# Performance work log

Hardware: AMD Instinct MI355X
Metric: run time of the kernel (lower is better)

## Reference

```python
import jax, jax.numpy as jnp
import numpy as np

N, E, F_IN, EDGE_DIM = 50000, 1600000, 128, 16
H, C = 4, 32            # heads, per-head channels for conv1/conv2
C_OUT = 2               # conv3: heads=1, out_channels=2
HC = H * C              # 128 = hidden_channels * heads
NEG_SLOPE = 0.2
BN_EPS = 1e-5


def setup_inputs() -> dict:
    key = jax.random.key(0)
    ks = jax.random.split(key, 40)
    rn = lambda k, s, sc: jax.random.normal(k, s, jnp.float32) * sc
    inp = {}
    inp["x"] = rn(ks[0], (N, F_IN), 1.0)
    inp["edge_index"] = jax.random.randint(ks[1], (2, E), 0, N, dtype=jnp.int32)
    inp["edge_attr"] = rn(ks[2], (E, EDGE_DIM), 1.0)
    # GATConv layer 1 (in=F_IN -> H x C)
    inp["W1"] = rn(ks[3], (F_IN, HC), F_IN ** -0.5)
    inp["as1"] = rn(ks[4], (H, C), 0.1)
    inp["ad1"] = rn(ks[5], (H, C), 0.1)
    inp["We1"] = rn(ks[6], (EDGE_DIM, HC), EDGE_DIM ** -0.5)
    inp["ae1"] = rn(ks[7], (H, C), 0.1)
    inp["b1"] = jnp.zeros((HC,), jnp.float32)
    # BN1 (eval mode: running stats)
    inp["g1"] = jnp.ones((HC,), jnp.float32)
    inp["be1"] = jnp.zeros((HC,), jnp.float32)
    inp["rm1"] = rn(ks[8], (HC,), 0.1)
    inp["rv1"] = jnp.ones((HC,), jnp.float32)
    # GATConv layer 2 (in=HC -> H x C)
    inp["W2"] = rn(ks[9], (HC, HC), HC ** -0.5)
    inp["as2"] = rn(ks[10], (H, C), 0.1)
    inp["ad2"] = rn(ks[11], (H, C), 0.1)
    inp["We2"] = rn(ks[12], (EDGE_DIM, HC), EDGE_DIM ** -0.5)
    inp["ae2"] = rn(ks[13], (H, C), 0.1)
    inp["b2"] = jnp.zeros((HC,), jnp.float32)
    inp["g2"] = jnp.ones((HC,), jnp.float32)
    inp["be2"] = jnp.zeros((HC,), jnp.float32)
    inp["rm2"] = rn(ks[14], (HC,), 0.1)
    inp["rv2"] = jnp.ones((HC,), jnp.float32)
    inp["W3"] = rn(ks[15], (HC, C_OUT), HC ** -0.5)
    inp["as3"] = rn(ks[16], (1, C_OUT), 0.1)
    inp["ad3"] = rn(ks[17], (1, C_OUT), 0.1)
    inp["We3"] = rn(ks[18], (EDGE_DIM, C_OUT), EDGE_DIM ** -0.5)
    inp["ae3"] = rn(ks[19], (1, C_OUT), 0.1)
    inp["b3"] = jnp.zeros((C_OUT,), jnp.float32)
    return inp


def _gat_layer(x, src, dst, eattr, W, a_s, a_d, We, a_e, b, heads, ch):
    """PyG GATConv (shared src/dst linear, edge_dim, add_self_loops already applied)."""
    n = x.shape[0]
    xp = (x @ W).reshape(n, heads, ch)                      # [N,H,C]
    alpha_src = (xp * a_s).sum(-1)                          # [N,H]
    alpha_dst = (xp * a_d).sum(-1)                          # [N,H]
    ep = (eattr @ We).reshape(-1, heads, ch)                # [E,H,C]
    alpha_e = (ep * a_e).sum(-1)                            # [E,H]
    alpha = alpha_src[src] + alpha_dst[dst] + alpha_e       # [E,H]
    alpha = jax.nn.leaky_relu(alpha, NEG_SLOPE)
    # segment softmax over incoming edges of each dst node
    m = jax.ops.segment_max(alpha, dst, num_segments=n)     # every node has a self loop
    ex = jnp.exp(alpha - m[dst])
    s = jax.ops.segment_sum(ex, dst, num_segments=n)
    alpha = ex / (s[dst] + 1e-16)                           # [E,H]
    msg = xp[src] * alpha[..., None]                        # [E,H,C]
    out = jax.ops.segment_sum(msg, dst, num_segments=n)     # [N,H,C]
    return out.reshape(n, heads * ch) + b


def _bn_eval(x, g, b, rm, rv):
    return (x - rm) * (g * jax.lax.rsqrt(rv + BN_EPS)) + b


def reference(x, edge_index, edge_attr,
              W1, as1, ad1, We1, ae1, b1, g1, be1, rm1, rv1,
              W2, as2, ad2, We2, ae2, b2, g2, be2, rm2, rv2,
              W3, as3, ad3, We3, ae3, b3):
    n = x.shape[0]
    loop = jnp.arange(n, dtype=edge_index.dtype)
    src = jnp.concatenate([edge_index[0], loop])
    dst = jnp.concatenate([edge_index[1], loop])
    # self-loop edge_attr fill_value='mean' (PyG default)
    ea_mean = jnp.broadcast_to(edge_attr.mean(0), (n, edge_attr.shape[1]))
    ea = jnp.concatenate([edge_attr, ea_mean], axis=0)

    h = _gat_layer(x, src, dst, ea, W1, as1, ad1, We1, ae1, b1, H, C)
    h = jax.nn.elu(_bn_eval(h, g1, be1, rm1, rv1))
    h = _gat_layer(h, src, dst, ea, W2, as2, ad2, We2, ae2, b2, H, C)
    h = jax.nn.elu(_bn_eval(h, g2, be2, rm2, rv2))
    out = _gat_layer(h, src, dst, ea, W3, as3, ad3, We3, ae3, b3, 1, C_OUT)
    return out
```

## Files before the change

kernel.cpp:

```cpp
#include <hip/hip_runtime.h>
#include <hip/hip_fp16.h>
#include <math.h>

#define NN 50000
#define EE 1600000
#define ETOT (EE + NN)
#define NEG_SLOPE 0.2f
#define BN_EPS 1e-5f
#define PAY_BLOCKS 1024
#define NPB 128
#define NBUCK ((NN + NPB - 1) / NPB)
#define CHUNK 8192
#define NCHUNK ((EE + CHUNK - 1) / CHUNK)


static __device__ inline unsigned pkh2(float a, float b) {
  __half ha = __float2half_rn(a), hb = __float2half_rn(b);
  unsigned short ua = *(unsigned short*)&ha, ub = *(unsigned short*)&hb;
  return ((unsigned)ub << 16) | ua;
}
static __device__ inline float upkh(unsigned u, int hi) {
  unsigned short s = hi ? (unsigned short)(u >> 16) : (unsigned short)(u & 0xffff);
  __half h = *(__half*)&s;
  return __half2float(h);
}

__global__ void compute_M_k(const float* __restrict__ We1, const float* __restrict__ ae1,
                            const float* __restrict__ We2, const float* __restrict__ ae2,
                            const float* __restrict__ We3, const float* __restrict__ ae3,
                            float* __restrict__ M) {
  int t = threadIdx.x;
  if (t < 64) {
    int d = t >> 2, h = t & 3;
    float s1 = 0.f, s2 = 0.f;
    for (int c = 0; c < 32; ++c) {
      s1 += We1[d * 128 + h * 32 + c] * ae1[h * 32 + c];
      s2 += We2[d * 128 + h * 32 + c] * ae2[h * 32 + c];
    }
    M[t] = s1;
    M[64 + t] = s2;
  }
  if (t < 16) {
    M[128 + t] = We3[t * 2] * ae3[0] + We3[t * 2 + 1] * ae3[1];
  }
}

__global__ __launch_bounds__(256) void payload_k(const int* __restrict__ src,
                                                 const float* __restrict__ ea,
                                                 const float* __restrict__ M,
                                                 uint4* __restrict__ payA,
                                                 uint2* __restrict__ payB,
                                                 float* __restrict__ mean_part) {
  __shared__ float sM[144];
  int t = threadIdx.x;
  if (t < 144) sM[t] = M[t];
  __syncthreads();
  float macc[16];
#pragma unroll
  for (int d = 0; d < 16; ++d) macc[d] = 0.f;

  for (int e = blockIdx.x * 256 + t; e < EE; e += PAY_BLOCKS * 256) {
    float v[16];
    const float4* p = (const float4*)(ea + (size_t)e * 16);
    float4 q0 = p[0], q1 = p[1], q2 = p[2], q3 = p[3];
    v[0] = q0.x; v[1] = q0.y; v[2] = q0.z; v[3] = q0.w;
    v[4] = q1.x; v[5] = q1.y; v[6] = q1.z; v[7] = q1.w;
    v[8] = q2.x; v[9] = q2.y; v[10] = q2.z; v[11] = q2.w;
    v[12] = q3.x; v[13] = q3.y; v[14] = q3.z; v[15] = q3.w;
    float a1[4], a2[4];
#pragma unroll
    for (int h = 0; h < 4; ++h) {
      float s1 = 0.f, s2 = 0.f;
#pragma unroll
      for (int d = 0; d < 16; ++d) {
        s1 += v[d] * sM[d * 4 + h];
        s2 += v[d] * sM[64 + d * 4 + h];
      }
      a1[h] = s1; a2[h] = s2;
    }
    float a3 = 0.f;
#pragma unroll
    for (int d = 0; d < 16; ++d) a3 += v[d] * sM[128 + d];
#pragma unroll
    for (int d = 0; d < 16; ++d) macc[d] += v[d];

    payA[e] = make_uint4(pkh2(a1[0], a1[1]), pkh2(a1[2], a1[3]),
                         pkh2(a2[0], a2[1]), pkh2(a2[2], a2[3]));
    payB[e] = make_uint2(__float_as_uint(a3), (unsigned)src[e]);
  }
#pragma unroll
  for (int d = 0; d < 16; ++d) {
#pragma unroll
    for (int off = 32; off; off >>= 1) macc[d] += __shfl_xor(macc[d], off, 64);
  }
  __shared__ float swsum[4][16];
  int w = t >> 6, l = t & 63;
  if (l == 0) {
#pragma unroll
    for (int d = 0; d < 16; ++d) swsum[w][d] = macc[d];
  }
  __syncthreads();
  if (t < 16) {
    mean_part[(size_t)blockIdx.x * 16 + t] =
        swsum[0][t] + swsum[1][t] + swsum[2][t] + swsum[3][t];
  }
}

__global__ __launch_bounds__(256) void selfloop_k(const float* __restrict__ mean_part,
                                                  const float* __restrict__ M,
                                                  float* __restrict__ alpha_sl) {
  __shared__ float s[256];
  int t = threadIdx.x;
  int d = t & 15, c = t >> 4;
  float v = 0.f;
  for (int i = c * 64; i < (c + 1) * 64; ++i) v += mean_part[(size_t)i * 16 + d];
  s[t] = v;
  __syncthreads();
  if (t < 16) {
    float sum = 0.f;
    for (int c2 = 0; c2 < 16; ++c2) sum += s[c2 * 16 + t];
    s[t] = sum / (float)EE;
  }
  __syncthreads();
  if (t < 9) {
    float r = 0.f;
    if (t < 4) {
      for (int dd = 0; dd < 16; ++dd) r += s[dd] * M[dd * 4 + t];
    } else if (t < 8) {
      int h = t - 4;
      for (int dd = 0; dd < 16; ++dd) r += s[dd] * M[64 + dd * 4 + h];
    } else {
      for (int dd = 0; dd < 16; ++dd) r += s[dd] * M[128 + dd];
    }
    alpha_sl[t] = r;
  }
}

__global__ __launch_bounds__(256) void bcount_k(const int* __restrict__ dst,
                                                int* __restrict__ bucketCnt) {
  __shared__ int hist[512];
  int t = threadIdx.x;
  for (int b = t; b < 512; b += 256) hist[b] = 0;
  __syncthreads();
  for (int e = (blockIdx.x * 256 + t) * 4; e < EE; e += gridDim.x * 1024) {
    int4 d4 = *(const int4*)&dst[e];
    atomicAdd(&hist[d4.x >> 7], 1);
    atomicAdd(&hist[d4.y >> 7], 1);
    atomicAdd(&hist[d4.z >> 7], 1);
    atomicAdd(&hist[d4.w >> 7], 1);
  }
  __syncthreads();
  for (int b = t; b < NBUCK; b += 256)
    if (hist[b]) atomicAdd(&bucketCnt[b], hist[b]);
}

__global__ __launch_bounds__(512) void bscan_k(const int* __restrict__ bucketCnt,
                                               int* __restrict__ pBase,
                                               int* __restrict__ rBase,
                                               int* __restrict__ bcur) {
  __shared__ int s1[512], s2[512];
  int t = threadIdx.x;
  int cnt = (t < NBUCK) ? bucketCnt[t] : 0;
  int nn = 0;
  if (t < NBUCK) {
    int n0 = t * NPB;
    nn = NN - n0; if (nn > NPB) nn = NPB;
  }
  s1[t] = cnt;
  s2[t] = cnt + nn;
  __syncthreads();
  for (int off = 1; off < 512; off <<= 1) {
    int a = (t >= off) ? s1[t - off] : 0;
    int b = (t >= off) ? s2[t - off] : 0;
    __syncthreads();
    s1[t] += a; s2[t] += b;
    __syncthreads();
  }
  if (t < NBUCK) {
    pBase[t] = s1[t] - cnt;
    rBase[t] = s2[t] - (cnt + nn);
    bcur[t] = s1[t] - cnt;
  }
  if (t == 0) { pBase[NBUCK] = EE; rBase[NBUCK] = ETOT; }
}

__global__ __launch_bounds__(256) void bscat_k(const int* __restrict__ dst,
                                               int* __restrict__ bcur,
                                               unsigned* __restrict__ pairs) {
  __shared__ int hist[512];
  __shared__ int ofs[512];
  int t = threadIdx.x;
  for (int c = blockIdx.x; c < NCHUNK; c += gridDim.x) {
    int cb = c * CHUNK;
    for (int b = t; b < 512; b += 256) hist[b] = 0;
    __syncthreads();
#pragma unroll
    for (int k = 0; k < 8; ++k) {
      int e = cb + k * 1024 + t * 4;
      if (e < EE) {
        int4 d4 = *(const int4*)&dst[e];
        atomicAdd(&hist[d4.x >> 7], 1);
        atomicAdd(&hist[d4.y >> 7], 1);
        atomicAdd(&hist[d4.z >> 7], 1);
        atomicAdd(&hist[d4.w >> 7], 1);
      }
    }
    __syncthreads();
    for (int b = t; b < NBUCK; b += 256) {
      int h = hist[b];
      ofs[b] = h ? atomicAdd(&bcur[b], h) : 0;
      hist[b] = 0;
    }
    __syncthreads();
#pragma unroll
    for (int k = 0; k < 8; ++k) {
      int e = cb + k * 1024 + t * 4;
      if (e < EE) {
        int4 d4 = *(const int4*)&dst[e];
        int dd[4] = {d4.x, d4.y, d4.z, d4.w};
#pragma unroll
        for (int j = 0; j < 4; ++j) {
          int b = dd[j] >> 7;
          int pos = ofs[b] + atomicAdd(&hist[b], 1);
          pairs[pos] = ((unsigned)(dd[j] & (NPB - 1)) << 21) | (unsigned)(e + j);
        }
      }
    }
    __syncthreads();
  }
}

__global__ __launch_bounds__(256) void cbuild_k(const int* __restrict__ pBase,
                                                const int* __restrict__ rBase,
                                                const unsigned* __restrict__ pairs,
                                                const uint4* __restrict__ payA,
                                                const uint2* __restrict__ payB,
                                                const float* __restrict__ asl,
                                                uint2* __restrict__ recAE1,
                                                uint2* __restrict__ recAE2,
                                                float* __restrict__ rec3,
                                                int* __restrict__ recSrc,
                                                int* __restrict__ row_ofs) {
  __shared__ int lcnt[NPB];
  __shared__ int ss[NPB];
  __shared__ int cur[NPB];
  int b = blockIdx.x;
  int t = threadIdx.x;
  int n0 = b * NPB;
  int n1 = n0 + NPB; if (n1 > NN) n1 = NN;
  int nn = n1 - n0;
  int pb = pBase[b], pe = pBase[b + 1];
  if (t < NPB) lcnt[t] = 0;
  __syncthreads();
  for (int i = pb + t; i < pe; i += 256) atomicAdd(&lcnt[pairs[i] >> 21], 1);
  __syncthreads();
  int v = (t < nn) ? (lcnt[t] + 1) : 0;
  if (t < NPB) ss[t] = v;
  __syncthreads();
  for (int off = 1; off < NPB; off <<= 1) {
    int a = (t >= off && t < NPB) ? ss[t - off] : 0;
    __syncthreads();
    if (t < NPB) ss[t] += a;
    __syncthreads();
  }
  uint2 a1s = make_uint2(pkh2(asl[0], asl[1]), pkh2(asl[2], asl[3]));
  uint2 a2s = make_uint2(pkh2(asl[4], asl[5]), pkh2(asl[6], asl[7]));
  float a3s = asl[8];
  int rb = rBase[b];
  if (t < nn) {
    int self = rb + ss[t] - v;
    row_ofs[n0 + t] = self;
    cur[t] = self + 1;
    recAE1[self] = a1s; recAE2[self] = a2s; rec3[self] = a3s; recSrc[self] = n0 + t;
  }
  if (b == NBUCK - 1 && t == 0) row_ofs[NN] = ETOT;
  __syncthreads();
  for (int i0 = pb + t; i0 < pe; i0 += 1024) {
    unsigned u[4];
    bool valid[4];
    uint4 pA[4]; uint2 pB[4];
    int pos[4];
#pragma unroll
    for (int k = 0; k < 4; ++k) {
      int i = i0 + k * 256;
      valid[k] = (i < pe);
      if (valid[k]) u[k] = pairs[i];
    }
#pragma unroll
    for (int k = 0; k < 4; ++k) {
      if (valid[k]) {
        int eid = u[k] & 0x1FFFFF;
        pA[k] = payA[eid];
        pB[k] = payB[eid];
        pos[k] = atomicAdd(&cur[u[k] >> 21], 1);
      }
    }
#pragma unroll
    for (int k = 0; k < 4; ++k) {
      if (valid[k]) {
        recAE1[pos[k]] = make_uint2(pA[k].x, pA[k].y);
        recAE2[pos[k]] = make_uint2(pA[k].z, pA[k].w);
        rec3[pos[k]] = __uint_as_float(pB[k].x);
        recSrc[pos[k]] = (int)pB[k].y;
      }
    }
  }
}

__global__ __launch_bounds__(256) void gemm128a_k(const float* __restrict__ X,
                                                  const float* __restrict__ W,
                                                  const float* __restrict__ as,
                                                  const float* __restrict__ ad,
                                                  __half* __restrict__ Y,
                                                  float* __restrict__ asrc,
                                                  float* __restrict__ adst,
                                                  int nrows) {
  __shared__ float sW[128 * 64];
  __shared__ float sX[64 * 132];
  __shared__ float sas[128], sad[128];
  int t = threadIdx.x;
  int r0 = blockIdx.x * 64;
  int cb = blockIdx.y;
  if (t < 128) { sas[t] = as[t]; sad[t] = ad[t]; }
#pragma unroll
  for (int i = 0; i < 8; ++i) {
    int flat = t + i * 256;
    int k = flat >> 4, c4 = flat & 15;
    *(float4*)&sW[k * 64 + c4 * 4] = *(const float4*)&W[k * 128 + cb * 64 + c4 * 4];
  }
  int rows = nrows - r0; if (rows > 64) rows = 64;
#pragma unroll
  for (int i = 0; i < 8; ++i) {
    int flat = t + i * 256;
    int r = flat >> 5, k4 = flat & 31;
    if (r < rows)
      *(float4*)&sX[r * 132 + k4 * 4] = *(const float4*)&X[(size_t)(r0 + r) * 128 + k4 * 4];
  }
  __syncthreads();
  int cq = t & 15, rl = t >> 4;
  float4 acc[4];
#pragma unroll
  for (int i = 0; i < 4; ++i) acc[i] = make_float4(0.f, 0.f, 0.f, 0.f);

  for (int k = 0; k < 128; k += 4) {
    float4 w0 = *(float4*)&sW[(k + 0) * 64 + cq * 4];
    float4 w1 = *(float4*)&sW[(k + 1) * 64 + cq * 4];
    float4 w2 = *(float4*)&sW[(k + 2) * 64 + cq * 4];
    float4 w3 = *(float4*)&sW[(k + 3) * 64 + cq * 4];
#pragma unroll
    for (int i = 0; i < 4; ++i) {
      float4 xv = *(float4*)&sX[(rl + i * 16) * 132 + k];
      acc[i].x += xv.x * w0.x + xv.y * w1.x + xv.z * w2.x + xv.w * w3.x;
      acc[i].y += xv.x * w0.y + xv.y * w1.y + xv.z * w2.y + xv.w * w3.y;
      acc[i].z += xv.x * w0.z + xv.y * w1.z + xv.z * w2.z + xv.w * w3.z;
      acc[i].w += xv.x * w0.w + xv.y * w1.w + xv.z * w2.w + xv.w * w3.w;
    }
  }
  int h = cb * 2 + (cq >> 3);
  int col0 = cb * 64 + cq * 4;
#pragma unroll
  for (int i = 0; i < 4; ++i) {
    int r = rl + i * 16;
    if (r < rows) {
      uint2 st;
      st.x = pkh2(acc[i].x, acc[i].y);
      st.y = pkh2(acc[i].z, acc[i].w);
      *(uint2*)&Y[(size_t)(r0 + r) * 128 + col0] = st;
      float s1 = acc[i].x * sas[col0] + acc[i].y * sas[col0 + 1] +
                 acc[i].z * sas[col0 + 2] + acc[i].w * sas[col0 + 3];
      float s2 = acc[i].x * sad[col0] + acc[i].y * sad[col0 + 1] +
                 acc[i].z * sad[col0 + 2] + acc[i].w * sad[col0 + 3];
      s1 += __shfl_xor(s1, 1, 8); s1 += __shfl_xor(s1, 2, 8); s1 += __shfl_xor(s1, 4, 8);
      s2 += __shfl_xor(s2, 1, 8); s2 += __shfl_xor(s2, 2, 8); s2 += __shfl_xor(s2, 4, 8);
      if ((cq & 7) == 0) {
        asrc[(size_t)(r0 + r) * 4 + h] = s1;
        adst[(size_t)(r0 + r) * 4 + h] = s2;
      }
    }
  }
}

__global__ __launch_bounds__(128) void agg128_k(
    const int* __restrict__ row_ofs, const unsigned* __restrict__ recAE,
    const int* __restrict__ recSrc, const __half* __restrict__ xp,
    const float* __restrict__ asrc, const float* __restrict__ adst,
    const float* __restrict__ bias, const float* __restrict__ g,
    const float* __restrict__ be, const float* __restrict__ rm,
    const float* __restrict__ rv, float* __restrict__ out) {
  int n = blockIdx.x;
  int t = threadIdx.x;
  int h = t >> 5, j = t & 31;
  int e4 = t >> 4, gg = t & 15;
  int hh = gg >> 2;
  __shared__ float s_w[4 * 64];
  __shared__ int s_src[64];
  __shared__ float sf[4], sden[4];
  __shared__ float sacc[8][132];
  int beg = row_ofs[n], end = row_ofs[n + 1];
  float adn = adst[(size_t)n * 4 + h];
  float m_run = -1e30f, s_run = 0.f;
  float acc[8];
#pragma unroll
  for (int i = 0; i < 8; ++i) acc[i] = 0.f;

  for (int base = beg; base < end; base += 64) {
    int cnt = end - base; if (cnt > 64) cnt = 64;
    float a0 = -1e30f, a1 = -1e30f;
    if (j < cnt) {
      int idx = base + j;
      float ae = upkh(recAE[(size_t)idx * 2 + (h >> 1)], h & 1);
      int sj = recSrc[idx];
      if (h == 0) s_src[j] = sj;
      float a = asrc[(size_t)sj * 4 + h] + adn + ae;
      a0 = (a > 0.f) ? a : NEG_SLOPE * a;
    }
    if (j + 32 < cnt) {
      int idx = base + j + 32;
      float ae = upkh(recAE[(size_t)idx * 2 + (h >> 1)], h & 1);
      int sj = recSrc[idx];
      if (h == 0) s_src[j + 32] = sj;
      float a = asrc[(size_t)sj * 4 + h] + adn + ae;
      a1 = (a > 0.f) ? a : NEG_SLOPE * a;
    }
    float cm = fmaxf(a0, a1);
#pragma unroll
    for (int off = 16; off; off >>= 1) cm = fmaxf(cm, __shfl_xor(cm, off, 32));
    float f = 1.f;
    if (cm > m_run) { f = expf(m_run - cm); s_run *= f; m_run = cm; }
    if (j == 0) sf[h] = f;
    float ex0 = (j < cnt) ? expf(a0 - m_run) : 0.f;
    float ex1 = (j + 32 < cnt) ? expf(a1 - m_run) : 0.f;
    s_w[h * 64 + j] = ex0;
    s_w[h * 64 + j + 32] = ex1;
    float se = ex0 + ex1;
#pragma unroll
    for (int off = 16; off; off >>= 1) se += __shfl_xor(se, off, 32);
    s_run += se;
    __syncthreads();
    float ff = sf[hh];
    if (ff != 1.f) {
#pragma unroll
      for (int i = 0; i < 8; ++i) acc[i] *= ff;
    }
    for (int e2 = 0; e2 < cnt; e2 += 16) {
      int ed0 = e2 + e4, ed1 = e2 + e4 + 8;
      bool b0 = ed0 < cnt, b1 = ed1 < cnt;
      uint4 v0, v1;
      float w0 = 0.f, w1 = 0.f;
      if (b0) {
        int s0 = s_src[ed0]; w0 = s_w[hh * 64 + ed0];
        v0 = *(const uint4*)&xp[(size_t)s0 * 128 + gg * 8];
      }
      if (b1) {
        int s1 = s_src[ed1]; w1 = s_w[hh * 64 + ed1];
        v1 = *(const uint4*)&xp[(size_t)s1 * 128 + gg * 8];
      }
      if (b0) {
        acc[0] += w0 * upkh(v0.x, 0); acc[1] += w0 * upkh(v0.x, 1);
        acc[2] += w0 * upkh(v0.y, 0); acc[3] += w0 * upkh(v0.y, 1);
        acc[4] += w0 * upkh(v0.z, 0); acc[5] += w0 * upkh(v0.z, 1);
        acc[6] += w0 * upkh(v0.w, 0); acc[7] += w0 * upkh(v0.w, 1);
      }
      if (b1) {
        acc[0] += w1 * upkh(v1.x, 0); acc[1] += w1 * upkh(v1.x, 1);
        acc[2] += w1 * upkh(v1.y, 0); acc[3] += w1 * upkh(v1.y, 1);
        acc[4] += w1 * upkh(v1.z, 0); acc[5] += w1 * upkh(v1.z, 1);
        acc[6] += w1 * upkh(v1.w, 0); acc[7] += w1 * upkh(v1.w, 1);
      }
    }
    __syncthreads();
  }
  if (j == 0) sden[h] = s_run;
#pragma unroll
  for (int i = 0; i < 8; ++i) sacc[e4][gg * 8 + i] = acc[i];
  __syncthreads();
  float v = 0.f;
#pragma unroll
  for (int i = 0; i < 8; ++i) v += sacc[i][t];
  v = v / (sden[t >> 5] + 1e-16f) + bias[t];
  v = (v - rm[t]) * (g[t] * rsqrtf(rv[t] + BN_EPS)) + be[t];
  v = (v > 0.f) ? v : (expf(v) - 1.f);
  out[(size_t)n * 128 + t] = v;
}

__global__ __launch_bounds__(256) void xp3_k(const float* __restrict__ h2,
                                             const float* __restrict__ W3,
                                             const float* __restrict__ as3,
                                             const float* __restrict__ ad3,
                                             float* __restrict__ xp3,
                                             float* __restrict__ asrc3,
                                             float* __restrict__ adst3) {
  __shared__ float sW[256];
  int t = threadIdx.x;
  sW[t] = W3[t];
  __syncthreads();
  int n = blockIdx.x * 256 + t;
  if (n < NN) {
    const float4* row = (const float4*)(h2 + (size_t)n * 128);
    float y0 = 0.f, y1 = 0.f;
#pragma unroll
    for (int i = 0; i < 32; ++i) {
      float4 v = row[i];
      y0 += v.x * sW[(i * 4 + 0) * 2] + v.y * sW[(i * 4 + 1) * 2] +
            v.z * sW[(i * 4 + 2) * 2] + v.w * sW[(i * 4 + 3) * 2];
      y1 += v.x * sW[(i * 4 + 0) * 2 + 1] + v.y * sW[(i * 4 + 1) * 2 + 1] +
            v.z * sW[(i * 4 + 2) * 2 + 1] + v.w * sW[(i * 4 + 3) * 2 + 1];
    }
    xp3[n * 2] = y0;
    xp3[n * 2 + 1] = y1;
    asrc3[n] = y0 * as3[0] + y1 * as3[1];
    adst3[n] = y0 * ad3[0] + y1 * ad3[1];
  }
}

__global__ __launch_bounds__(256) void agg2_k(const int* __restrict__ row_ofs,
                                              const float* __restrict__ rec3,
                                              const int* __restrict__ recSrc,
                                              const float* __restrict__ xp3,
                                              const float* __restrict__ asrc3,
                                              const float* __restrict__ adst3,
                                              const float* __restrict__ b3,
                                              float* __restrict__ out) {
  int t = threadIdx.x;
  int w = t >> 6, l = t & 63;
  int n = blockIdx.x * 4 + w;
  if (n >= NN) return;
  int beg = row_ofs[n], end = row_ofs[n + 1];
  float adn = adst3[n];
  float m = -1e30f, s = 0.f, a0 = 0.f, a1 = 0.f;
  for (int idx = beg + l; idx < end; idx += 64) {
    float aev = rec3[idx];
    int sj = recSrc[idx];
    float a = asrc3[sj] + adn + aev;
    a = (a > 0.f) ? a : NEG_SLOPE * a;
    if (a > m) {
      float f = expf(m - a);
      s *= f; a0 *= f; a1 *= f; m = a;
    }
    float ex = expf(a - m);
    s += ex;
    a0 += ex * xp3[sj * 2];
    a1 += ex * xp3[sj * 2 + 1];
  }
  float M = m;
#pragma unroll
  for (int off = 32; off; off >>= 1) M = fmaxf(M, __shfl_xor(M, off, 64));
  float f = expf(m - M);
  s *= f; a0 *= f; a1 *= f;
#pragma unroll
  for (int off = 32; off; off >>= 1) {
    s += __shfl_xor(s, off, 64);
    a0 += __shfl_xor(a0, off, 64);
    a1 += __shfl_xor(a1, off, 64);
  }
  if (l == 0) {
    float inv = 1.f / (s + 1e-16f);
    out[n * 2] = a0 * inv + b3[0];
    out[n * 2 + 1] = a1 * inv + b3[1];
  }
}

extern "C" void kernel_launch(void* const* d_in, const int* in_sizes, int n_in,
                              void* d_out, int out_size, void* d_ws, size_t ws_size,
                              hipStream_t stream) {
  const float* x   = (const float*)d_in[0];
  const int*   ei  = (const int*)d_in[1];
  const float* ea  = (const float*)d_in[2];
  const float* W1  = (const float*)d_in[3];
  const float* as1 = (const float*)d_in[4];
  const float* ad1 = (const float*)d_in[5];
  const float* We1 = (const float*)d_in[6];
  const float* ae1 = (const float*)d_in[7];
  const float* b1  = (const float*)d_in[8];
  const float* g1  = (const float*)d_in[9];
  const float* be1 = (const float*)d_in[10];
  const float* rm1 = (const float*)d_in[11];
  const float* rv1 = (const float*)d_in[12];
  const float* W2  = (const float*)d_in[13];
  const float* as2 = (const float*)d_in[14];
  const float* ad2 = (const float*)d_in[15];
  const float* We2 = (const float*)d_in[16];
  const float* ae2 = (const float*)d_in[17];
  const float* b2  = (const float*)d_in[18];
  const float* g2  = (const float*)d_in[19];
  const float* be2 = (const float*)d_in[20];
  const float* rm2 = (const float*)d_in[21];
  const float* rv2 = (const float*)d_in[22];
  const float* W3  = (const float*)d_in[23];
  const float* as3 = (const float*)d_in[24];
  const float* ad3 = (const float*)d_in[25];
  const float* We3 = (const float*)d_in[26];
  const float* ae3 = (const float*)d_in[27];
  const float* b3  = (const float*)d_in[28];

  const int* srcA = ei;
  const int* dstA = ei + EE;

  char* p = (char*)d_ws;
  auto alloc = [&](size_t bytes) -> void* {
    void* r = (void*)p;
    p += (bytes + 255) & ~(size_t)255;
    return r;
  };
  uint4* payA   = (uint4*)alloc(sizeof(uint4) * (size_t)EE);
  uint2* payB   = (uint2*)alloc(sizeof(uint2) * (size_t)EE);
  uint2* recAE1 = (uint2*)alloc(sizeof(uint2) * (size_t)ETOT);
  uint2* recAE2 = (uint2*)alloc(sizeof(uint2) * (size_t)ETOT);
  float* rec3   = (float*)alloc(sizeof(float) * (size_t)ETOT);
  int*   recSrc = (int*)alloc(sizeof(int) * (size_t)ETOT);
  unsigned* pairs = (unsigned*)alloc(sizeof(unsigned) * (size_t)EE);
  __half* xp    = (__half*)alloc(sizeof(__half) * (size_t)NN * 128);
  float* hbuf   = (float*)alloc(sizeof(float) * (size_t)NN * 128);
  float* Mbuf   = (float*)alloc(sizeof(float) * 144);
  float* meanp  = (float*)alloc(sizeof(float) * (size_t)PAY_BLOCKS * 16);
  float* asl    = (float*)alloc(sizeof(float) * 12);
  float* asrc   = (float*)alloc(sizeof(float) * (size_t)NN * 4);
  float* adst   = (float*)alloc(sizeof(float) * (size_t)NN * 4);
  float* xp3    = (float*)alloc(sizeof(float) * (size_t)NN * 2);
  float* asrc3  = (float*)alloc(sizeof(float) * (size_t)NN);
  float* adst3  = (float*)alloc(sizeof(float) * (size_t)NN);
  int* bucketCnt = (int*)alloc(sizeof(int) * (size_t)NBUCK);
  int* pBase    = (int*)alloc(sizeof(int) * (size_t)(NBUCK + 1));
  int* rBase    = (int*)alloc(sizeof(int) * (size_t)(NBUCK + 1));
  int* bcur     = (int*)alloc(sizeof(int) * (size_t)NBUCK);
  int* row_ofs  = (int*)alloc(sizeof(int) * (size_t)(NN + 1));

  hipMemsetAsync(bucketCnt, 0, NBUCK * sizeof(int), stream);

  compute_M_k<<<1, 64, 0, stream>>>(We1, ae1, We2, ae2, We3, ae3, Mbuf);
  payload_k<<<PAY_BLOCKS, 256, 0, stream>>>(srcA, ea, Mbuf, payA, payB, meanp);
  selfloop_k<<<1, 256, 0, stream>>>(meanp, Mbuf, asl);
  bcount_k<<<256, 256, 0, stream>>>(dstA, bucketCnt);
  bscan_k<<<1, 512, 0, stream>>>(bucketCnt, pBase, rBase, bcur);
  bscat_k<<<200, 256, 0, stream>>>(dstA, bcur, pairs);
  cbuild_k<<<NBUCK, 256, 0, stream>>>(pBase, rBase, pairs, payA, payB, asl,
                                      recAE1, recAE2, rec3, recSrc, row_ofs);

  gemm128a_k<<<dim3((NN + 63) / 64, 2), 256, 0, stream>>>(x, W1, as1, ad1, xp, asrc, adst, NN);
  agg128_k<<<NN, 128, 0, stream>>>(row_ofs, (const unsigned*)recAE1, recSrc, xp,
                                   asrc, adst, b1, g1, be1, rm1, rv1, hbuf);
  gemm128a_k<<<dim3((NN + 63) / 64, 2), 256, 0, stream>>>(hbuf, W2, as2, ad2, xp, asrc, adst, NN);
  agg128_k<<<NN, 128, 0, stream>>>(row_ofs, (const unsigned*)recAE2, recSrc, xp,
                                   asrc, adst, b2, g2, be2, rm2, rv2, hbuf);
  xp3_k<<<(NN + 255) / 256, 256, 0, stream>>>(hbuf, W3, as3, ad3, xp3, asrc3, adst3);
  agg2_k<<<(NN + 3) / 4, 256, 0, stream>>>(row_ofs, rec3, recSrc, xp3, asrc3, adst3,
                                           b3, (float*)d_out);
}
```

Before: 409.3 us.

## Compute edge attention payload in CSR build instead of separate payload pass

Removes the payload kernel that wrote per-edge packed attention terms to intermediate arrays. The edge-attribute mean and the bucket histogram are now fused into one pass, and cbuild gathers the raw 16-float edge attributes and computes the attention terms on the fly. The src index is carried through the scatter pairs, and buckets shrink to 64 nodes to get more cbuild blocks. This cuts the payload write and reread traffic, but cbuild now does random 64-byte gathers of edge_attr instead of 24-byte payload reads.

After: 398.4 us. -2.7%, faster.

```diff
diff --git a/kernel.cpp b/kernel.cpp
--- a/kernel.cpp
+++ b/kernel.cpp
@@ -8,7 +8,7 @@
 #define NEG_SLOPE 0.2f
 #define BN_EPS 1e-5f
 #define PAY_BLOCKS 1024
-#define NPB 128
+#define NPB 64
 #define NBUCK ((NN + NPB - 1) / NPB)
 #define CHUNK 8192
 #define NCHUNK ((EE + CHUNK - 1) / CHUNK)
@@ -45,48 +45,25 @@
   }
 }
 
-__global__ __launch_bounds__(256) void payload_k(const int* __restrict__ src,
-                                                 const float* __restrict__ ea,
-                                                 const float* __restrict__ M,
-                                                 uint4* __restrict__ payA,
-                                                 uint2* __restrict__ payB,
-                                                 float* __restrict__ mean_part) {
-  __shared__ float sM[144];
-  int t = threadIdx.x;
-  if (t < 144) sM[t] = M[t];
+__global__ __launch_bounds__(256) void bcount_k(const int* __restrict__ dst,
+                                                const float* __restrict__ ea,
+                                                int* __restrict__ bucketCnt,
+                                                float* __restrict__ mean_part) {
+  __shared__ int hist[1024];
+  int t = threadIdx.x;
+  for (int b = t; b < 1024; b += 256) hist[b] = 0;
   __syncthreads();
   float macc[16];
 #pragma unroll
   for (int d = 0; d < 16; ++d) macc[d] = 0.f;
-
   for (int e = blockIdx.x * 256 + t; e < EE; e += PAY_BLOCKS * 256) {
-    float v[16];
     const float4* p = (const float4*)(ea + (size_t)e * 16);
     float4 q0 = p[0], q1 = p[1], q2 = p[2], q3 = p[3];
-    v[0] = q0.x; v[1] = q0.y; v[2] = q0.z; v[3] = q0.w;
-    v[4] = q1.x; v[5] = q1.y; v[6] = q1.z; v[7] = q1.w;
-    v[8] = q2.x; v[9] = q2.y; v[10] = q2.z; v[11] = q2.w;
-    v[12] = q3.x; v[13] = q3.y; v[14] = q3.z; v[15] = q3.w;
-    float a1[4], a2[4];
-#pragma unroll
-    for (int h = 0; h < 4; ++h) {
-      float s1 = 0.f, s2 = 0.f;
-#pragma unroll
-      for (int d = 0; d < 16; ++d) {
-        s1 += v[d] * sM[d * 4 + h];
-        s2 += v[d] * sM[64 + d * 4 + h];
-      }
-      a1[h] = s1; a2[h] = s2;
-    }
-    float a3 = 0.f;
-#pragma unroll
-    for (int d = 0; d < 16; ++d) a3 += v[d] * sM[128 + d];
-#pragma unroll
-    for (int d = 0; d < 16; ++d) macc[d] += v[d];
-
-    payA[e] = make_uint4(pkh2(a1[0], a1[1]), pkh2(a1[2], a1[3]),
-                         pkh2(a2[0], a2[1]), pkh2(a2[2], a2[3]));
-    payB[e] = make_uint2(__float_as_uint(a3), (unsigned)src[e]);
+    macc[0] += q0.x; macc[1] += q0.y; macc[2] += q0.z; macc[3] += q0.w;
+    macc[4] += q1.x; macc[5] += q1.y; macc[6] += q1.z; macc[7] += q1.w;
+    macc[8] += q2.x; macc[9] += q2.y; macc[10] += q2.z; macc[11] += q2.w;
+    macc[12] += q3.x; macc[13] += q3.y; macc[14] += q3.z; macc[15] += q3.w;
+    atomicAdd(&hist[dst[e] >> 6], 1);
   }
 #pragma unroll
   for (int d = 0; d < 16; ++d) {
@@ -104,6 +81,8 @@
     mean_part[(size_t)blockIdx.x * 16 + t] =
         swsum[0][t] + swsum[1][t] + swsum[2][t] + swsum[3][t];
   }
+  for (int b = t; b < NBUCK; b += 256)
+    if (hist[b]) atomicAdd(&bucketCnt[b], hist[b]);
 }
 
 __global__ __launch_bounds__(256) void selfloop_k(const float* __restrict__ mean_part,
@@ -136,29 +115,11 @@
   }
 }
 
-__global__ __launch_bounds__(256) void bcount_k(const int* __restrict__ dst,
-                                                int* __restrict__ bucketCnt) {
-  __shared__ int hist[512];
-  int t = threadIdx.x;
-  for (int b = t; b < 512; b += 256) hist[b] = 0;
-  __syncthreads();
-  for (int e = (blockIdx.x * 256 + t) * 4; e < EE; e += gridDim.x * 1024) {
-    int4 d4 = *(const int4*)&dst[e];
-    atomicAdd(&hist[d4.x >> 7], 1);
-    atomicAdd(&hist[d4.y >> 7], 1);
-    atomicAdd(&hist[d4.z >> 7], 1);
-    atomicAdd(&hist[d4.w >> 7], 1);
-  }
-  __syncthreads();
-  for (int b = t; b < NBUCK; b += 256)
-    if (hist[b]) atomicAdd(&bucketCnt[b], hist[b]);
-}
-
-__global__ __launch_bounds__(512) void bscan_k(const int* __restrict__ bucketCnt,
-                                               int* __restrict__ pBase,
-                                               int* __restrict__ rBase,
-                                               int* __restrict__ bcur) {
-  __shared__ int s1[512], s2[512];
+__global__ __launch_bounds__(1024) void bscan_k(const int* __restrict__ bucketCnt,
+                                                int* __restrict__ pBase,
+                                                int* __restrict__ rBase,
+                                                int* __restrict__ bcur) {
+  __shared__ int s1[1024], s2[1024];
   int t = threadIdx.x;
   int cnt = (t < NBUCK) ? bucketCnt[t] : 0;
   int nn = 0;
@@ -169,7 +130,7 @@
   s1[t] = cnt;
   s2[t] = cnt + nn;
   __syncthreads();
-  for (int off = 1; off < 512; off <<= 1) {
+  for (int off = 1; off < 1024; off <<= 1) {
     int a = (t >= off) ? s1[t - off] : 0;
     int b = (t >= off) ? s2[t - off] : 0;
     __syncthreads();
@@ -185,24 +146,25 @@
 }
 
 __global__ __launch_bounds__(256) void bscat_k(const int* __restrict__ dst,
+                                               const int* __restrict__ src,
                                                int* __restrict__ bcur,
-                                               unsigned* __restrict__ pairs) {
-  __shared__ int hist[512];
-  __shared__ int ofs[512];
+                                               uint2* __restrict__ pairs) {
+  __shared__ int hist[1024];
+  __shared__ int ofs[1024];
   int t = threadIdx.x;
   for (int c = blockIdx.x; c < NCHUNK; c += gridDim.x) {
     int cb = c * CHUNK;
-    for (int b = t; b < 512; b += 256) hist[b] = 0;
+    for (int b = t; b < 1024; b += 256) hist[b] = 0;
     __syncthreads();
 #pragma unroll
     for (int k = 0; k < 8; ++k) {
       int e = cb + k * 1024 + t * 4;
       if (e < EE) {
         int4 d4 = *(const int4*)&dst[e];
-        atomicAdd(&hist[d4.x >> 7], 1);
-        atomicAdd(&hist[d4.y >> 7], 1);
-        atomicAdd(&hist[d4.z >> 7], 1);
-        atomicAdd(&hist[d4.w >> 7], 1);
+        atomicAdd(&hist[d4.x >> 6], 1);
+        atomicAdd(&hist[d4.y >> 6], 1);
+        atomicAdd(&hist[d4.z >> 6], 1);
+        atomicAdd(&hist[d4.w >> 6], 1);
       }
     }
     __syncthreads();
@@ -217,12 +179,15 @@
       int e = cb + k * 1024 + t * 4;
       if (e < EE) {
         int4 d4 = *(const int4*)&dst[e];
+        int4 s4 = *(const int4*)&src[e];
         int dd[4] = {d4.x, d4.y, d4.z, d4.w};
+        int sv[4] = {s4.x, s4.y, s4.z, s4.w};
 #pragma unroll
         for (int j = 0; j < 4; ++j) {
-          int b = dd[j] >> 7;
+          int b = dd[j] >> 6;
           int pos = ofs[b] + atomicAdd(&hist[b], 1);
-          pairs[pos] = ((unsigned)(dd[j] & (NPB - 1)) << 21) | (unsigned)(e + j);
+          pairs[pos] = make_uint2(((unsigned)(dd[j] & (NPB - 1)) << 21) | (unsigned)(e + j),
+                                  (unsigned)sv[j]);
         }
       }
     }
@@ -232,27 +197,29 @@
 
 __global__ __launch_bounds__(256) void cbuild_k(const int* __restrict__ pBase,
                                                 const int* __restrict__ rBase,
-                                                const unsigned* __restrict__ pairs,
-                                                const uint4* __restrict__ payA,
-                                                const uint2* __restrict__ payB,
+                                                const uint2* __restrict__ pairs,
+                                                const float* __restrict__ ea,
+                                                const float* __restrict__ M,
                                                 const float* __restrict__ asl,
                                                 uint2* __restrict__ recAE1,
                                                 uint2* __restrict__ recAE2,
                                                 float* __restrict__ rec3,
                                                 int* __restrict__ recSrc,
                                                 int* __restrict__ row_ofs) {
+  __shared__ float sM[144];
   __shared__ int lcnt[NPB];
   __shared__ int ss[NPB];
   __shared__ int cur[NPB];
   int b = blockIdx.x;
   int t = threadIdx.x;
+  if (t < 144) sM[t] = M[t];
+  if (t < NPB) lcnt[t] = 0;
+  __syncthreads();
   int n0 = b * NPB;
   int n1 = n0 + NPB; if (n1 > NN) n1 = NN;
   int nn = n1 - n0;
   int pb = pBase[b], pe = pBase[b + 1];
-  if (t < NPB) lcnt[t] = 0;
-  __syncthreads();
-  for (int i = pb + t; i < pe; i += 256) atomicAdd(&lcnt[pairs[i] >> 21], 1);
+  for (int i = pb + t; i < pe; i += 256) atomicAdd(&lcnt[pairs[i].x >> 21], 1);
   __syncthreads();
   int v = (t < nn) ? (lcnt[t] + 1) : 0;
   if (t < NPB) ss[t] = v;
@@ -263,23 +230,22 @@
     if (t < NPB) ss[t] += a;
     __syncthreads();
   }
-  uint2 a1s = make_uint2(pkh2(asl[0], asl[1]), pkh2(asl[2], asl[3]));
-  uint2 a2s = make_uint2(pkh2(asl[4], asl[5]), pkh2(asl[6], asl[7]));
-  float a3s = asl[8];
   int rb = rBase[b];
   if (t < nn) {
     int self = rb + ss[t] - v;
     row_ofs[n0 + t] = self;
     cur[t] = self + 1;
-    recAE1[self] = a1s; recAE2[self] = a2s; rec3[self] = a3s; recSrc[self] = n0 + t;
+    recAE1[self] = make_uint2(pkh2(asl[0], asl[1]), pkh2(asl[2], asl[3]));
+    recAE2[self] = make_uint2(pkh2(asl[4], asl[5]), pkh2(asl[6], asl[7]));
+    rec3[self] = asl[8];
+    recSrc[self] = n0 + t;
   }
   if (b == NBUCK - 1 && t == 0) row_ofs[NN] = ETOT;
   __syncthreads();
   for (int i0 = pb + t; i0 < pe; i0 += 1024) {
-    unsigned u[4];
+    uint2 u[4];
     bool valid[4];
-    uint4 pA[4]; uint2 pB[4];
-    int pos[4];
+    float4 q[4][4];
 #pragma unroll
     for (int k = 0; k < 4; ++k) {
       int i = i0 + k * 256;
@@ -289,19 +255,37 @@
 #pragma unroll
     for (int k = 0; k < 4; ++k) {
       if (valid[k]) {
-        int eid = u[k] & 0x1FFFFF;
-        pA[k] = payA[eid];
-        pB[k] = payB[eid];
-        pos[k] = atomicAdd(&cur[u[k] >> 21], 1);
+        const float4* p = (const float4*)(ea + (size_t)(u[k].x & 0x1FFFFF) * 16);
+        q[k][0] = p[0]; q[k][1] = p[1]; q[k][2] = p[2]; q[k][3] = p[3];
       }
     }
 #pragma unroll
     for (int k = 0; k < 4; ++k) {
       if (valid[k]) {
-        recAE1[pos[k]] = make_uint2(pA[k].x, pA[k].y);
-        recAE2[pos[k]] = make_uint2(pA[k].z, pA[k].w);
-        rec3[pos[k]] = __uint_as_float(pB[k].x);
-        recSrc[pos[k]] = (int)pB[k].y;
+        float vv[16];
+        vv[0] = q[k][0].x; vv[1] = q[k][0].y; vv[2] = q[k][0].z; vv[3] = q[k][0].w;
+        vv[4] = q[k][1].x; vv[5] = q[k][1].y; vv[6] = q[k][1].z; vv[7] = q[k][1].w;
+        vv[8] = q[k][2].x; vv[9] = q[k][2].y; vv[10] = q[k][2].z; vv[11] = q[k][2].w;
+        vv[12] = q[k][3].x; vv[13] = q[k][3].y; vv[14] = q[k][3].z; vv[15] = q[k][3].w;
+        float a1[4], a2[4];
+#pragma unroll
+        for (int h = 0; h < 4; ++h) {
+          float s1 = 0.f, s2 = 0.f;
+#pragma unroll
+          for (int d = 0; d < 16; ++d) {
+            s1 += vv[d] * sM[d * 4 + h];
+            s2 += vv[d] * sM[64 + d * 4 + h];
+          }
+          a1[h] = s1; a2[h] = s2;
+        }
+        float a3 = 0.f;
+#pragma unroll
+        for (int d = 0; d < 16; ++d) a3 += vv[d] * sM[128 + d];
+        int pos = atomicAdd(&cur[u[k].x >> 21], 1);
+        recAE1[pos] = make_uint2(pkh2(a1[0], a1[1]), pkh2(a1[2], a1[3]));
+        recAE2[pos] = make_uint2(pkh2(a2[0], a2[1]), pkh2(a2[2], a2[3]));
+        rec3[pos] = a3;
+        recSrc[pos] = (int)u[k].y;
       }
     }
   }
@@ -602,13 +586,11 @@
     p += (bytes + 255) & ~(size_t)255;
     return r;
   };
-  uint4* payA   = (uint4*)alloc(sizeof(uint4) * (size_t)EE);
-  uint2* payB   = (uint2*)alloc(sizeof(uint2) * (size_t)EE);
   uint2* recAE1 = (uint2*)alloc(sizeof(uint2) * (size_t)ETOT);
   uint2* recAE2 = (uint2*)alloc(sizeof(uint2) * (size_t)ETOT);
   float* rec3   = (float*)alloc(sizeof(float) * (size_t)ETOT);
   int*   recSrc = (int*)alloc(sizeof(int) * (size_t)ETOT);
-  unsigned* pairs = (unsigned*)alloc(sizeof(unsigned) * (size_t)EE);
+  uint2* pairs  = (uint2*)alloc(sizeof(uint2) * (size_t)EE);
   __half* xp    = (__half*)alloc(sizeof(__half) * (size_t)NN * 128);
   float* hbuf   = (float*)alloc(sizeof(float) * (size_t)NN * 128);
   float* Mbuf   = (float*)alloc(sizeof(float) * 144);
@@ -628,12 +610,11 @@
   hipMemsetAsync(bucketCnt, 0, NBUCK * sizeof(int), stream);
 
   compute_M_k<<<1, 64, 0, stream>>>(We1, ae1, We2, ae2, We3, ae3, Mbuf);
-  payload_k<<<PAY_BLOCKS, 256, 0, stream>>>(srcA, ea, Mbuf, payA, payB, meanp);
+  bcount_k<<<PAY_BLOCKS, 256, 0, stream>>>(dstA, ea, bucketCnt, meanp);
   selfloop_k<<<1, 256, 0, stream>>>(meanp, Mbuf, asl);
-  bcount_k<<<256, 256, 0, stream>>>(dstA, bucketCnt);
-  bscan_k<<<1, 512, 0, stream>>>(bucketCnt, pBase, rBase, bcur);
-  bscat_k<<<200, 256, 0, stream>>>(dstA, bcur, pairs);
-  cbuild_k<<<NBUCK, 256, 0, stream>>>(pBase, rBase, pairs, payA, payB, asl,
+  bscan_k<<<1, 1024, 0, stream>>>(bucketCnt, pBase, rBase, bcur);
+  bscat_k<<<200, 256, 0, stream>>>(dstA, srcA, bcur, pairs);
+  cbuild_k<<<NBUCK, 256, 0, stream>>>(pBase, rBase, pairs, ea, Mbuf, asl,
                                       recAE1, recAE2, rec3, recSrc, row_ofs);
 
   gemm128a_k<<<dim3((NN + 63) / 64, 2), 256, 0, stream>>>(x, W1, as1, ad1, xp, asrc, adst, NN);
```
